# Kernel optimization log

Hardware: AMD Instinct MI355X
Metric: run time of the kernel (lower is better)

The kernel has to match this reference:

```python
import jax, jax.numpy as jnp
import numpy as np

B, T, F, H = 64, 256, 64, 512  # batch, seq_len, temporal_feature_num, hidden_size_lstm


def setup_inputs() -> dict:
    key = jax.random.key(0)
    ks = jax.random.split(key, 8)
    return {
        "temporal_features": jax.random.normal(ks[0], (B, T, F), dtype=jnp.float32),
        "temporal_masks": jax.random.uniform(ks[1], (B, T, F), dtype=jnp.float32),
        "h0": jax.random.normal(ks[2], (F, B, H), dtype=jnp.float32),
        "c0": jax.random.normal(ks[3], (F, B, H), dtype=jnp.float32),
        "W_ih": jax.random.normal(ks[4], (F, 4 * H, 2), dtype=jnp.float32) * 0.05,
        "W_hh": jax.random.normal(ks[5], (F, 4 * H, H), dtype=jnp.float32) * 0.05,
        "b_ih": jax.random.normal(ks[6], (F, 4 * H), dtype=jnp.float32) * 0.05,
        "b_hh": jax.random.normal(ks[7], (F, 4 * H), dtype=jnp.float32) * 0.05,
    }


def reference(temporal_features, temporal_masks, h0, c0, W_ih, W_hh, b_ih, b_hh):
    # x: [T, F, B, 2] -- per feature, the LSTM input is (feature_value, mask)
    x = jnp.stack([temporal_features, temporal_masks], axis=-1)  # [B, T, F, 2]
    x = jnp.transpose(x, (1, 2, 0, 3))  # [T, F, B, 2]

    bias = (b_ih + b_hh)[:, None, :]  # [F, 1, 4H]

    def step(carry, x_t):
        h, c = carry  # each [F, B, H]
        gates = (jnp.einsum('fbi,fgi->fbg', x_t, W_ih)
                 + jnp.einsum('fbh,fgh->fbg', h, W_hh)
                 + bias)  # [F, B, 4H]
        i_g, f_g, g_g, o_g = jnp.split(gates, 4, axis=-1)  # torch LSTMCell gate order i,f,g,o
        i_g = jax.nn.sigmoid(i_g)
        f_g = jax.nn.sigmoid(f_g)
        g_g = jnp.tanh(g_g)
        o_g = jax.nn.sigmoid(o_g)
        c_new = f_g * c + i_g * g_g
        h_new = o_g * jnp.tanh(c_new)
        return (h_new, c_new), None

    (h_final, _), _ = jax.lax.scan(step, (h0, c0), x)
    return h_final  # [F, B, H] -- stacked version of the returned h_list
```

## Files before the change

kernel.cpp:

```cpp
#include <hip/hip_runtime.h>
#include <hip/hip_bf16.h>
#include <stdint.h>

#define F_N 64
#define T_N 256
#define B_N 64
#define H_N 512
#define STREAM_KS 8
#define VREG_KS0 8
#define NVSTAT 6
#define LDS_KS0 14

typedef __attribute__((ext_vector_type(8))) __bf16 bf16x8;
typedef __attribute__((ext_vector_type(4))) float f32x4;
typedef __attribute__((ext_vector_type(4))) uint32_t u32x4;


__global__ void pack_x_kernel(const float* __restrict__ tf, const float* __restrict__ tm,
                              float* __restrict__ xp) {
  int tid = blockIdx.x * 256 + threadIdx.x;
  if (tid >= T_N * B_N * F_N) return;
  int f = tid & 63;
  int b = (tid >> 6) & 63;
  int t = tid >> 12;
  float v = tf[((size_t)b * T_N + t) * F_N + f];
  float m = tm[((size_t)b * T_N + t) * F_N + f];
  float* dst = xp + (((size_t)t * F_N + f) * B_N + b) * 2;
  dst[0] = v;
  dst[1] = m;
}

__global__ void pack_h0_kernel(const float* __restrict__ h0, __bf16* __restrict__ hx0) {
  int tid = blockIdx.x * 256 + threadIdx.x;
  if (tid < F_N * B_N * H_N) hx0[tid] = (__bf16)h0[tid];
}

__global__ void pack_w_kernel(const float* __restrict__ Whh, __bf16* __restrict__ Wp) {
  int gtid = blockIdx.x * 256 + threadIdx.x;
  int lane = gtid & 63;
  int nt = (gtid >> 6) & 3;
  int ks = (gtid >> 8) & 15;
  int w = (gtid >> 12) & 7;
  int q = (gtid >> 15) & 3;
  int f = gtid >> 17;
  int l15 = lane & 15, lhi = lane >> 4;
  int n_local = w * 64 + nt * 16 + l15;
  int r_local = n_local >> 2;
  int gam = n_local & 3;
  int grow = gam * 512 + q * 128 + r_local;
  const float* src = Whh + ((size_t)f * 2048 + grow) * 512 + ks * 32 + lhi * 8;
  float4 u0 = *(const float4*)src;
  float4 u1 = *(const float4*)(src + 4);
  bf16x8 v;
  v[0] = (__bf16)u0.x; v[1] = (__bf16)u0.y; v[2] = (__bf16)u0.z; v[3] = (__bf16)u0.w;
  v[4] = (__bf16)u1.x; v[5] = (__bf16)u1.y; v[6] = (__bf16)u1.z; v[7] = (__bf16)u1.w;
  *(bf16x8*)((char*)Wp + (size_t)gtid * 16) = v;
}


__global__ void __launch_bounds__(512, 1) __attribute__((amdgpu_waves_per_eu(2, 2)))
lstm_main(
    const float* __restrict__ c0, const __bf16* __restrict__ Wp,
    const float* __restrict__ Wih, const float* __restrict__ bih,
    const float* __restrict__ bhh, const float* __restrict__ xp,
    __bf16* hx, unsigned int* barr, unsigned int* xcdmap, float* __restrict__ out) {
  const int blk = blockIdx.x;
  const int f = blk & 63;
  const int q = blk >> 6;
  const int tid = threadIdx.x;
  const int lane = tid & 63;
  const int w = tid >> 6;
  const int l15 = lane & 15;
  const int lhi = lane >> 4;
  const int ls = lane & 3;
  const int lr = l15 >> 2;

  __shared__ __align__(16) unsigned char lds_h[65536];
  __shared__ __align__(16) unsigned char lds_stage[16384];
  __shared__ __align__(16) unsigned char lds_wst[65536];
  __shared__ __align__(16) float ldsB[512];
  __shared__ __align__(16) float lds0[512];
  __shared__ __align__(16) float lds1[512];
  __shared__ int s_same;

  {
    int i = tid;
    int r = i >> 2, g = i & 3;
    int row = g * 512 + q * 128 + r;
    size_t ro = (size_t)f * 2048 + row;
    ldsB[i] = bih[ro] + bhh[ro];
    lds0[i] = Wih[ro * 2 + 0];
    lds1[i] = Wih[ro * 2 + 1];
  }

  if (tid == 0) {
    uint32_t xcc;
    asm volatile("s_getreg_b32 %0, hwreg(HW_REG_XCC_ID)" : "=s"(xcc));
    xcc &= 15u;
    __hip_atomic_store(&xcdmap[f * 4 + q], xcc + 1u, __ATOMIC_RELAXED,
                       __HIP_MEMORY_SCOPE_AGENT);
    uint32_t ids[4];
    int ok = 1;
    for (int j = 0; j < 4; ++j) {
      unsigned int it = 0;
      uint32_t v;
      do {
        v = __hip_atomic_load(&xcdmap[f * 4 + j], __ATOMIC_RELAXED,
                              __HIP_MEMORY_SCOPE_AGENT);
        if (++it > 2000000u) { ok = 0; break; }
        if (v == 0u) __builtin_amdgcn_s_sleep(2);
      } while (v == 0u);
      ids[j] = v;
    }
    if (ok) ok = (ids[0] == ids[1]) & (ids[1] == ids[2]) & (ids[2] == ids[3]);
    s_same = ok;
  }

  const bf16x8* wpbase = (const bf16x8*)Wp + ((size_t)((f * 4 + q) * 8 + w)) * 4096 + lane;

  bf16x8 s[3][4];
#define LOAD_SLOT(SL, KS)                                       \
  {                                                             \
    _Pragma("unroll") for (int nt_ = 0; nt_ < 4; ++nt_)         \
        s[SL][nt_] = wpbase[((KS) * 4 + nt_) * 64];             \
  }

  bf16x8 wsf[NVSTAT][4];
#pragma unroll
  for (int s2 = 0; s2 < NVSTAT; ++s2)
#pragma unroll
    for (int nt = 0; nt < 4; ++nt) wsf[s2][nt] = wpbase[((VREG_KS0 + s2) * 4 + nt) * 64];

#pragma unroll
  for (int ksi = 0; ksi < 2; ++ksi)
#pragma unroll
    for (int nt = 0; nt < 4; ++nt) {
      bf16x8 v = wpbase[((LDS_KS0 + ksi) * 4 + nt) * 64];
      *(bf16x8*)(lds_wst + (((ksi * 8 + w) * 4 + nt) << 10) + lane * 16) = v;
    }

  float c_reg[4][4];
#pragma unroll
  for (int mt = 0; mt < 4; ++mt) {
    int brow = mt * 16 + lhi * 4 + ls;
#pragma unroll
    for (int nt = 0; nt < 4; ++nt) {
      int rg = w * 16 + nt * 4 + lr;
      c_reg[mt][nt] = c0[((size_t)f * B_N + brow) * H_N + q * 128 + rg];
    }
  }

  const size_t hxfeat = (size_t)f * (B_N * H_N);
  const size_t hxstride = (size_t)F_N * B_N * H_N;

  {
    const unsigned char* src = (const unsigned char*)(hx + hxfeat);
    uint32_t b = tid >> 3;
    uint32_t off = (tid & 7) * 32;
    uint32_t sw = (b & 7) << 4;
#pragma unroll
    for (int qq = 0; qq < 4; ++qq) {
      uint32_t gb = b * 1024 + qq * 256 + off;
      uint4 u0 = *(const uint4*)(src + gb);
      uint4 u1 = *(const uint4*)(src + gb + 16);
      *(uint4*)(lds_h + (gb ^ sw)) = u0;
      *(uint4*)(lds_h + ((gb + 16) ^ sw)) = u1;
    }
  }
  LOAD_SLOT(0, 0);
  LOAD_SLOT(1, 1);
  LOAD_SLOT(2, 2);
  __syncthreads();
  const bool fastpath = (s_same != 0);

#define READ_A(KS)                                                                     \
  {                                                                                    \
    _Pragma("unroll") for (int mt = 0; mt < 4; ++mt) {                                 \
      int row = mt * 16 + l15;                                                         \
      uint32_t byteoff =                                                               \
          (uint32_t)(row * 1024) + (((uint32_t)((KS) * 64 + lhi * 16)) ^ ((row & 7) << 4)); \
      a[mt] = *(const bf16x8*)(lds_h + byteoff);                                       \
    }                                                                                  \
  }
#define MFMA_W(WARR)                                                                   \
  {                                                                                    \
    _Pragma("unroll") for (int mt = 0; mt < 4; ++mt)                                   \
        _Pragma("unroll") for (int nt = 0; nt < 4; ++nt)                               \
            acc[mt][nt] = __builtin_amdgcn_mfma_f32_16x16x32_bf16(a[mt], (WARR)[nt],   \
                                                                  acc[mt][nt], 0, 0, 0); \
  }
#define STATIC_V(S2) { READ_A(VREG_KS0 + (S2)); MFMA_W(wsf[S2]); }
#define STATIC_L(KSI)                                                                  \
  {                                                                                    \
    READ_A(LDS_KS0 + (KSI));                                                           \
    bf16x8 wfrag[4];                                                                   \
    _Pragma("unroll") for (int nt = 0; nt < 4; ++nt) wfrag[nt] =                       \
        *(const bf16x8*)(lds_wst + ((((KSI) * 8 + w) * 4 + nt) << 10) + lane * 16);    \
    MFMA_W(wfrag);                                                                     \
  }
#define STREAM(POS)                                                                    \
  {                                                                                    \
    const int ks_ = ((POS) + par4) & 7;                                                \
    READ_A(ks_);                                                                       \
    MFMA_W(s[(POS) % 3]);                                                              \
    if ((POS) + 3 < STREAM_KS) {                                                       \
      const int ksn_ = ((POS) + 3 + par4) & 7;                                         \
      _Pragma("unroll") for (int nt_ = 0; nt_ < 4; ++nt_)                              \
          s[(POS) % 3][nt_] = wpbase[(ksn_ * 4 + nt_) * 64];                           \
    }                                                                                  \
  }

#pragma unroll 1
  for (int t = 0; t < T_N; ++t) {
    const int par4 = (t & 1) << 2;
    const int par4n = ((t + 1) & 1) << 2;
    f32x4 acc[4][4] = {};
    bf16x8 a[4];

    STATIC_V(0); STREAM(0);
    STATIC_V(1); STREAM(1);
    STATIC_V(2); STREAM(2);
    STATIC_V(3); STREAM(3);
    STATIC_V(4); STREAM(4);
    STATIC_V(5); STREAM(5);
    STATIC_L(0); STREAM(6);
    STATIC_L(1); STREAM(7);

    const bool last = (t == T_N - 1);
    const float* xpt = xp + (((size_t)t * F_N + f) * B_N) * 2;
#pragma unroll
    for (int mt = 0; mt < 4; ++mt) {
      int brow = mt * 16 + lhi * 4 + ls;
      float xv = xpt[brow * 2];
      float xm = xpt[brow * 2 + 1];
#pragma unroll
      for (int nt = 0; nt < 4; ++nt) {
        float v0 = acc[mt][nt][0], v1 = acc[mt][nt][1], v2 = acc[mt][nt][2], v3 = acc[mt][nt][3];
        {
          float t0 = __shfl_xor(v0, 1), t1 = __shfl_xor(v1, 1),
                t2 = __shfl_xor(v2, 1), t3 = __shfl_xor(v3, 1);
          if (lane & 1) { v0 = t1; v2 = t3; } else { v1 = t0; v3 = t2; }
        }
        {
          float t0 = __shfl_xor(v0, 2), t1 = __shfl_xor(v1, 2),
                t2 = __shfl_xor(v2, 2), t3 = __shfl_xor(v3, 2);
          if (lane & 2) { v0 = t2; v1 = t3; } else { v2 = t0; v3 = t1; }
        }
        int rg = w * 16 + nt * 4 + lr;
        int idx4 = rg << 2;
        float4 tb = *(const float4*)&ldsB[idx4];
        float4 w0t = *(const float4*)&lds0[idx4];
        float4 w1t = *(const float4*)&lds1[idx4];
        v0 += tb.x + w0t.x * xv + w1t.x * xm;
        v1 += tb.y + w0t.y * xv + w1t.y * xm;
        v2 += tb.z + w0t.z * xv + w1t.z * xm;
        v3 += tb.w + w0t.w * xv + w1t.w * xm;
        float ig = __builtin_amdgcn_rcpf(1.0f + __expf(-v0));
        float fg = __builtin_amdgcn_rcpf(1.0f + __expf(-v1));
        float gg = 2.0f * __builtin_amdgcn_rcpf(1.0f + __expf(-2.0f * v2)) - 1.0f;
        float og = __builtin_amdgcn_rcpf(1.0f + __expf(-v3));
        float cn = fg * c_reg[mt][nt] + ig * gg;
        c_reg[mt][nt] = cn;
        float th = 2.0f * __builtin_amdgcn_rcpf(1.0f + __expf(-2.0f * cn)) - 1.0f;
        float hn = og * th;
        if (last) {
          out[((size_t)f * B_N + brow) * H_N + q * 128 + rg] = hn;
        } else {
          uint32_t sw = (uint32_t)((brow & 7) << 4);
          *(__bf16*)(lds_stage + ((uint32_t)(brow * 256 + rg * 2) ^ sw)) = (__bf16)hn;
        }
      }
    }
    if (last) break;

    __syncthreads();

    {
      __bf16* dstbuf = hx + ((size_t)((t + 1) & 1)) * hxstride + hxfeat;
      uint32_t b = tid >> 3;
      uint32_t off = (tid & 7) * 32;
      uint32_t sw = (b & 7) << 4;
      u32x4 u0 = *(const u32x4*)(lds_stage + ((b * 256 + off) ^ sw));
      u32x4 u1 = *(const u32x4*)(lds_stage + ((b * 256 + off + 16) ^ sw));
      unsigned char* dp = (unsigned char*)dstbuf + b * 1024 + q * 256 + off;
      if (fastpath) {
        asm volatile("global_store_dwordx4 %0, %1, off sc0" ::"v"(dp), "v"(u0) : "memory");
        asm volatile("global_store_dwordx4 %0, %1, off sc0" ::"v"(dp + 16), "v"(u1) : "memory");
        asm volatile("s_waitcnt vmcnt(0)" ::: "memory");
      } else {
        *(u32x4*)(dp) = u0;
        *(u32x4*)(dp + 16) = u1;
      }
      uint32_t hb = b * 1024 + q * 256 + off;
      *(u32x4*)(lds_h + (hb ^ sw)) = u0;
      *(u32x4*)(lds_h + ((hb + 16) ^ sw)) = u1;
    }
    __syncthreads();

    if (tid == 0) {
      unsigned int* bp = barr + f * T_N + t;
      if (fastpath)
        __hip_atomic_fetch_add(bp, 1u, __ATOMIC_RELAXED, __HIP_MEMORY_SCOPE_AGENT);
      else
        __hip_atomic_fetch_add(bp, 1u, __ATOMIC_RELEASE, __HIP_MEMORY_SCOPE_AGENT);
    }
    LOAD_SLOT(0, (0 + par4n) & 7);
    LOAD_SLOT(1, (1 + par4n) & 7);
    LOAD_SLOT(2, (2 + par4n) & 7);
    if (tid == 0) {
      unsigned int* bp = barr + f * T_N + t;
      unsigned int it = 0;
      while (__hip_atomic_load(bp, __ATOMIC_RELAXED, __HIP_MEMORY_SCOPE_AGENT) < 4u) {
        __builtin_amdgcn_s_sleep(1);
        if (++it > 4000000u) break;
      }
      if (!fastpath)
        (void)__hip_atomic_load(bp, __ATOMIC_ACQUIRE, __HIP_MEMORY_SCOPE_AGENT);
    }
    __syncthreads();

    if (fastpath) {
      asm volatile("buffer_inv sc0" ::: "memory");
    }
    {
      const unsigned char* src =
          (const unsigned char*)(hx + ((size_t)((t + 1) & 1)) * hxstride + hxfeat);
      uint32_t b = tid >> 3;
      uint32_t off = (tid & 7) * 32;
      uint32_t sw = (b & 7) << 4;
#pragma unroll
      for (int qq = 0; qq < 4; ++qq) {
        if (qq == q) continue;
        uint32_t gb = b * 1024 + qq * 256 + off;
        uint4 u0 = *(const uint4*)(src + gb);
        uint4 u1 = *(const uint4*)(src + gb + 16);
        *(uint4*)(lds_h + (gb ^ sw)) = u0;
        *(uint4*)(lds_h + ((gb + 16) ^ sw)) = u1;
      }
    }
    __syncthreads();
  }
#undef LOAD_SLOT
#undef READ_A
#undef MFMA_W
#undef STATIC_V
#undef STATIC_L
#undef STREAM
}

extern "C" void kernel_launch(void* const* d_in, const int* in_sizes, int n_in,
                              void* d_out, int out_size, void* d_ws, size_t ws_size,
                              hipStream_t stream) {
  const float* tf = (const float*)d_in[0];
  const float* tm = (const float*)d_in[1];
  const float* h0 = (const float*)d_in[2];
  const float* c0 = (const float*)d_in[3];
  const float* Wih = (const float*)d_in[4];
  const float* Whh = (const float*)d_in[5];
  const float* bih = (const float*)d_in[6];
  const float* bhh = (const float*)d_in[7];
  float* out = (float*)d_out;

  const size_t WP_BYTES = (size_t)8388608 * 16;
  const size_t XP_BYTES = (size_t)T_N * F_N * B_N * 2 * 4;
  const size_t HX_BYTES = (size_t)2 * F_N * B_N * H_N * 2;
  const size_t BARR_BYTES = (size_t)F_N * T_N * 4;
  const size_t MAP_BYTES = 1024;
  if (ws_size < WP_BYTES + XP_BYTES + HX_BYTES + BARR_BYTES + MAP_BYTES) return;

  char* ws = (char*)d_ws;
  __bf16* Wp = (__bf16*)ws;
  float* xp = (float*)(ws + WP_BYTES);
  __bf16* hx = (__bf16*)(ws + WP_BYTES + XP_BYTES);
  unsigned int* barr = (unsigned int*)(ws + WP_BYTES + XP_BYTES + HX_BYTES);
  unsigned int* xcdmap = (unsigned int*)(ws + WP_BYTES + XP_BYTES + HX_BYTES + BARR_BYTES);

  hipMemsetAsync(barr, 0, BARR_BYTES + MAP_BYTES, stream);
  pack_x_kernel<<<(T_N * B_N * F_N + 255) / 256, 256, 0, stream>>>(tf, tm, xp);
  pack_h0_kernel<<<(F_N * B_N * H_N + 255) / 256, 256, 0, stream>>>(h0, hx);
  pack_w_kernel<<<8388608 / 256, 256, 0, stream>>>(Whh, Wp);
  lstm_main<<<256, 512, 0, stream>>>(c0, Wp, Wih, bih, bhh, xp, hx, barr, xcdmap, out);
}
```

Baseline: 6.142 ms.

## Add per-XCD lockstep barrier and reverse stream k-slice order on odd steps

Adds an extra per-XCD barrier after the per-feature barrier. Each XCD with exactly 32 resident blocks waits until all of them finish the timestep, so the blocks that share that XCD's L2 stream the same weight slices together. The streamed k-slice order now changes from a rotation by 4 to an XOR with 7 on odd steps, so slices last used in the previous step are touched first. This aims to improve L2 hit rate for the streamed weights. It adds a cross-block wait per step that can stall on the slowest block.

```diff
diff --git a/kernel.cpp b/kernel.cpp
--- a/kernel.cpp
+++ b/kernel.cpp
@@ -63,7 +63,8 @@
     const float* __restrict__ c0, const __bf16* __restrict__ Wp,
     const float* __restrict__ Wih, const float* __restrict__ bih,
     const float* __restrict__ bhh, const float* __restrict__ xp,
-    __bf16* hx, unsigned int* barr, unsigned int* xcdmap, float* __restrict__ out) {
+    __bf16* hx, unsigned int* barr, unsigned int* xcdmap, unsigned int* xbar,
+    float* __restrict__ out) {
   const int blk = blockIdx.x;
   const int f = blk & 63;
   const int q = blk >> 6;
@@ -82,6 +83,8 @@
   __shared__ __align__(16) float lds0[512];
   __shared__ __align__(16) float lds1[512];
   __shared__ int s_same;
+  __shared__ int s_xt;
+  __shared__ int s_xcc;
 
   {
     int i = tid;
@@ -114,6 +117,25 @@
     }
     if (ok) ok = (ids[0] == ids[1]) & (ids[1] == ids[2]) & (ids[2] == ids[3]);
     s_same = ok;
+    int xt = 0;
+    if (ok) {
+      int good = 1, cnt = 0;
+      for (int j2 = 0; j2 < 256; ++j2) {
+        unsigned int it2 = 0;
+        uint32_t v2;
+        do {
+          v2 = __hip_atomic_load(&xcdmap[j2], __ATOMIC_RELAXED,
+                                 __HIP_MEMORY_SCOPE_AGENT);
+          if (v2 == 0u) __builtin_amdgcn_s_sleep(2);
+          if (++it2 > 2000000u) { good = 0; break; }
+        } while (v2 == 0u);
+        if (!good) break;
+        cnt += (v2 == xcc + 1u);
+      }
+      if (good && cnt == 32) xt = 32;
+    }
+    s_xt = xt;
+    s_xcc = (int)xcc;
   }
 
   const bf16x8* wpbase = (const bf16x8*)Wp + ((size_t)((f * 4 + q) * 8 + w)) * 4096 + lane;
@@ -172,6 +194,8 @@
   LOAD_SLOT(2, 2);
   __syncthreads();
   const bool fastpath = (s_same != 0);
+  int xsync = s_xt;
+  const int myxcc = s_xcc;
 
 #define READ_A(KS)                                                                     \
   {                                                                                    \
@@ -200,11 +224,11 @@
   }
 #define STREAM(POS)                                                                    \
   {                                                                                    \
-    const int ks_ = ((POS) + par4) & 7;                                                \
+    const int ks_ = (POS) ^ smask;                                                     \
     READ_A(ks_);                                                                       \
     MFMA_W(s[(POS) % 3]);                                                              \
     if ((POS) + 3 < STREAM_KS) {                                                       \
-      const int ksn_ = ((POS) + 3 + par4) & 7;                                         \
+      const int ksn_ = ((POS) + 3) ^ smask;                                            \
       _Pragma("unroll") for (int nt_ = 0; nt_ < 4; ++nt_)                              \
           s[(POS) % 3][nt_] = wpbase[(ksn_ * 4 + nt_) * 64];                           \
     }                                                                                  \
@@ -212,8 +236,8 @@
 
 #pragma unroll 1
   for (int t = 0; t < T_N; ++t) {
-    const int par4 = (t & 1) << 2;
-    const int par4n = ((t + 1) & 1) << 2;
+    const int smask = (t & 1) ? 7 : 0;
+    const int smaskn = ((t + 1) & 1) ? 7 : 0;
     f32x4 acc[4][4] = {};
     bf16x8 a[4];
 
@@ -304,9 +328,9 @@
       else
         __hip_atomic_fetch_add(bp, 1u, __ATOMIC_RELEASE, __HIP_MEMORY_SCOPE_AGENT);
     }
-    LOAD_SLOT(0, (0 + par4n) & 7);
-    LOAD_SLOT(1, (1 + par4n) & 7);
-    LOAD_SLOT(2, (2 + par4n) & 7);
+    LOAD_SLOT(0, 0 ^ smaskn);
+    LOAD_SLOT(1, 1 ^ smaskn);
+    LOAD_SLOT(2, 2 ^ smaskn);
     if (tid == 0) {
       unsigned int* bp = barr + f * T_N + t;
       unsigned int it = 0;
@@ -316,6 +340,15 @@
       }
       if (!fastpath)
         (void)__hip_atomic_load(bp, __ATOMIC_ACQUIRE, __HIP_MEMORY_SCOPE_AGENT);
+      if (xsync) {
+        unsigned int* xb = xbar + ((unsigned int)myxcc) * T_N + t;
+        __hip_atomic_fetch_add(xb, 1u, __ATOMIC_RELAXED, __HIP_MEMORY_SCOPE_AGENT);
+        unsigned int it3 = 0;
+        while (__hip_atomic_load(xb, __ATOMIC_RELAXED, __HIP_MEMORY_SCOPE_AGENT) < 32u) {
+          __builtin_amdgcn_s_sleep(1);
+          if (++it3 > 1000000u) { xsync = 0; break; }
+        }
+      }
     }
     __syncthreads();
 
@@ -366,7 +399,9 @@
   const size_t HX_BYTES = (size_t)2 * F_N * B_N * H_N * 2;
   const size_t BARR_BYTES = (size_t)F_N * T_N * 4;
   const size_t MAP_BYTES = 1024;
-  if (ws_size < WP_BYTES + XP_BYTES + HX_BYTES + BARR_BYTES + MAP_BYTES) return;
+  const size_t XBAR_BYTES = (size_t)8 * T_N * 4;
+  if (ws_size < WP_BYTES + XP_BYTES + HX_BYTES + BARR_BYTES + MAP_BYTES + XBAR_BYTES)
+    return;
 
   char* ws = (char*)d_ws;
   __bf16* Wp = (__bf16*)ws;
@@ -374,10 +409,12 @@
   __bf16* hx = (__bf16*)(ws + WP_BYTES + XP_BYTES);
   unsigned int* barr = (unsigned int*)(ws + WP_BYTES + XP_BYTES + HX_BYTES);
   unsigned int* xcdmap = (unsigned int*)(ws + WP_BYTES + XP_BYTES + HX_BYTES + BARR_BYTES);
-
-  hipMemsetAsync(barr, 0, BARR_BYTES + MAP_BYTES, stream);
+  unsigned int* xbar =
+      (unsigned int*)(ws + WP_BYTES + XP_BYTES + HX_BYTES + BARR_BYTES + MAP_BYTES);
+
+  hipMemsetAsync(barr, 0, BARR_BYTES + MAP_BYTES + XBAR_BYTES, stream);
   pack_x_kernel<<<(T_N * B_N * F_N + 255) / 256, 256, 0, stream>>>(tf, tm, xp);
   pack_h0_kernel<<<(F_N * B_N * H_N + 255) / 256, 256, 0, stream>>>(h0, hx);
   pack_w_kernel<<<8388608 / 256, 256, 0, stream>>>(Whh, Wp);
-  lstm_main<<<256, 512, 0, stream>>>(c0, Wp, Wih, bih, bhh, xp, hx, barr, xcdmap, out);
+  lstm_main<<<256, 512, 0, stream>>>(c0, Wp, Wih, bih, bhh, xp, hx, barr, xcdmap, xbar, out);
 }
```

Result: slower. 7.858 ms (+27.9%).

## Overlap own-quarter K-units of next step's GEMM with cross-block barrier wait

Applied to the files above, without the earlier changes.

Renumbers the K-units per block so each block's first units cover the hidden-state quarter it computed itself. Four of those MFMA steps (EARLY4) now run for the next timestep before waiting on the cross-block barrier and loading the other quarters of h. The aim is to hide the barrier spin and global h exchange behind useful matrix work. The cost is that the accumulators stay live across the barrier, which adds register pressure. The weight-to-unit mapping also has to remain consistent with the packed weight layout.

```diff
diff --git a/kernel.cpp b/kernel.cpp
--- a/kernel.cpp
+++ b/kernel.cpp
@@ -6,10 +6,8 @@
 #define T_N 256
 #define B_N 64
 #define H_N 512
-#define STREAM_KS 8
-#define VREG_KS0 8
 #define NVSTAT 6
-#define LDS_KS0 14
+#define NSTREAM 8
 
 typedef __attribute__((ext_vector_type(8))) __bf16 bf16x8;
 typedef __attribute__((ext_vector_type(4))) float f32x4;
@@ -74,6 +72,9 @@
   const int lhi = lane >> 4;
   const int ls = lane & 3;
   const int lr = l15 >> 2;
+  const int uq = q << 2;
+
+#define UNITJ(J) ((uq + (J)) & 15)
 
   __shared__ __align__(16) unsigned char lds_h[65536];
   __shared__ __align__(16) unsigned char lds_stage[16384];
@@ -119,25 +120,30 @@
   const bf16x8* wpbase = (const bf16x8*)Wp + ((size_t)((f * 4 + q) * 8 + w)) * 4096 + lane;
 
   bf16x8 s[3][4];
-#define LOAD_SLOT(SL, KS)                                       \
-  {                                                             \
-    _Pragma("unroll") for (int nt_ = 0; nt_ < 4; ++nt_)         \
-        s[SL][nt_] = wpbase[((KS) * 4 + nt_) * 64];             \
+#define LOAD_SLOT(SL, P, PAR)                                       \
+  {                                                                 \
+    const int u_ = UNITJ(8 + (((P) + (PAR)) & 7));                  \
+    _Pragma("unroll") for (int nt_ = 0; nt_ < 4; ++nt_)             \
+        s[SL][nt_] = wpbase[(u_ * 4 + nt_) * 64];                   \
   }
 
   bf16x8 wsf[NVSTAT][4];
 #pragma unroll
-  for (int s2 = 0; s2 < NVSTAT; ++s2)
-#pragma unroll
-    for (int nt = 0; nt < 4; ++nt) wsf[s2][nt] = wpbase[((VREG_KS0 + s2) * 4 + nt) * 64];
-
-#pragma unroll
-  for (int ksi = 0; ksi < 2; ++ksi)
+  for (int s2 = 0; s2 < NVSTAT; ++s2) {
+    const int u_ = UNITJ(s2);
+#pragma unroll
+    for (int nt = 0; nt < 4; ++nt) wsf[s2][nt] = wpbase[(u_ * 4 + nt) * 64];
+  }
+
+#pragma unroll
+  for (int ksi = 0; ksi < 2; ++ksi) {
+    const int u_ = UNITJ(6 + ksi);
 #pragma unroll
     for (int nt = 0; nt < 4; ++nt) {
-      bf16x8 v = wpbase[((LDS_KS0 + ksi) * 4 + nt) * 64];
+      bf16x8 v = wpbase[(u_ * 4 + nt) * 64];
       *(bf16x8*)(lds_wst + (((ksi * 8 + w) * 4 + nt) << 10) + lane * 16) = v;
     }
+  }
 
   float c_reg[4][4];
 #pragma unroll
@@ -167,18 +173,18 @@
       *(uint4*)(lds_h + ((gb + 16) ^ sw)) = u1;
     }
   }
-  LOAD_SLOT(0, 0);
-  LOAD_SLOT(1, 1);
-  LOAD_SLOT(2, 2);
+  LOAD_SLOT(0, 0, 0);
+  LOAD_SLOT(1, 1, 0);
+  LOAD_SLOT(2, 2, 0);
   __syncthreads();
   const bool fastpath = (s_same != 0);
 
-#define READ_A(KS)                                                                     \
+#define READ_A(U)                                                                      \
   {                                                                                    \
     _Pragma("unroll") for (int mt = 0; mt < 4; ++mt) {                                 \
       int row = mt * 16 + l15;                                                         \
       uint32_t byteoff =                                                               \
-          (uint32_t)(row * 1024) + (((uint32_t)((KS) * 64 + lhi * 16)) ^ ((row & 7) << 4)); \
+          (uint32_t)(row * 1024) + (((uint32_t)((U) * 64 + lhi * 16)) ^ ((row & 7) << 4)); \
       a[mt] = *(const bf16x8*)(lds_h + byteoff);                                       \
     }                                                                                  \
   }
@@ -189,10 +195,10 @@
             acc[mt][nt] = __builtin_amdgcn_mfma_f32_16x16x32_bf16(a[mt], (WARR)[nt],   \
                                                                   acc[mt][nt], 0, 0, 0); \
   }
-#define STATIC_V(S2) { READ_A(VREG_KS0 + (S2)); MFMA_W(wsf[S2]); }
+#define STATIC_V(S2) { READ_A(UNITJ(S2)); MFMA_W(wsf[S2]); }
 #define STATIC_L(KSI)                                                                  \
   {                                                                                    \
-    READ_A(LDS_KS0 + (KSI));                                                           \
+    READ_A(UNITJ(6 + (KSI)));                                                          \
     bf16x8 wfrag[4];                                                                   \
     _Pragma("unroll") for (int nt = 0; nt < 4; ++nt) wfrag[nt] =                       \
         *(const bf16x8*)(lds_wst + ((((KSI) * 8 + w) * 4 + nt) << 10) + lane * 16);    \
@@ -200,31 +206,71 @@
   }
 #define STREAM(POS)                                                                    \
   {                                                                                    \
-    const int ks_ = ((POS) + par4) & 7;                                                \
-    READ_A(ks_);                                                                       \
+    const int u_ = UNITJ(8 + (((POS) + par4) & 7));                                    \
+    READ_A(u_);                                                                        \
     MFMA_W(s[(POS) % 3]);                                                              \
-    if ((POS) + 3 < STREAM_KS) {                                                       \
-      const int ksn_ = ((POS) + 3 + par4) & 7;                                         \
+    if ((POS) + 3 < NSTREAM) {                                                         \
+      const int un_ = UNITJ(8 + (((POS) + 3 + par4) & 7));                             \
       _Pragma("unroll") for (int nt_ = 0; nt_ < 4; ++nt_)                              \
-          s[(POS) % 3][nt_] = wpbase[(ksn_ * 4 + nt_) * 64];                           \
+          s[(POS) % 3][nt_] = wpbase[(un_ * 4 + nt_) * 64];                            \
     }                                                                                  \
   }
+#define ACC_CLEAR                                                                      \
+  {                                                                                    \
+    _Pragma("unroll") for (int mt = 0; mt < 4; ++mt)                                   \
+        _Pragma("unroll") for (int nt = 0; nt < 4; ++nt)                               \
+            acc[mt][nt] = (f32x4){0.0f, 0.0f, 0.0f, 0.0f};                             \
+  }
+#define EARLY4 { STATIC_V(0); STATIC_V(1); STATIC_V(2); STATIC_V(3); }
+
+  f32x4 acc[4][4] = {};
+  bf16x8 a[4];
+  EARLY4;
 
 #pragma unroll 1
   for (int t = 0; t < T_N; ++t) {
     const int par4 = (t & 1) << 2;
     const int par4n = ((t + 1) & 1) << 2;
-    f32x4 acc[4][4] = {};
-    bf16x8 a[4];
-
-    STATIC_V(0); STREAM(0);
-    STATIC_V(1); STREAM(1);
-    STATIC_V(2); STREAM(2);
-    STATIC_V(3); STREAM(3);
-    STATIC_V(4); STREAM(4);
-    STATIC_V(5); STREAM(5);
-    STATIC_L(0); STREAM(6);
-    STATIC_L(1); STREAM(7);
+
+    if (t > 0) {
+      if (tid == 0) {
+        unsigned int* bp = barr + f * T_N + (t - 1);
+        unsigned int it = 0;
+        while (__hip_atomic_load(bp, __ATOMIC_RELAXED, __HIP_MEMORY_SCOPE_AGENT) < 4u) {
+          __builtin_amdgcn_s_sleep(1);
+          if (++it > 4000000u) break;
+        }
+        if (!fastpath)
+          (void)__hip_atomic_load(bp, __ATOMIC_ACQUIRE, __HIP_MEMORY_SCOPE_AGENT);
+      }
+      __syncthreads();
+      if (fastpath) {
+        asm volatile("buffer_inv sc0" ::: "memory");
+      }
+      {
+        const unsigned char* src =
+            (const unsigned char*)(hx + ((size_t)(t & 1)) * hxstride + hxfeat);
+        uint32_t b = tid >> 3;
+        uint32_t off = (tid & 7) * 32;
+        uint32_t sw = (b & 7) << 4;
+#pragma unroll
+        for (int qq = 0; qq < 4; ++qq) {
+          if (qq == q) continue;
+          uint32_t gb = b * 1024 + qq * 256 + off;
+          uint4 u0 = *(const uint4*)(src + gb);
+          uint4 u1 = *(const uint4*)(src + gb + 16);
+          *(uint4*)(lds_h + (gb ^ sw)) = u0;
+          *(uint4*)(lds_h + ((gb + 16) ^ sw)) = u1;
+        }
+      }
+      __syncthreads();
+    }
+
+    STATIC_V(4); STREAM(0);
+    STATIC_V(5); STREAM(1);
+    STATIC_L(0); STREAM(2);
+    STATIC_L(1); STREAM(3);
+    STREAM(4); STREAM(5); STREAM(6); STREAM(7);
 
     const bool last = (t == T_N - 1);
     const float* xpt = xp + (((size_t)t * F_N + f) * B_N) * 2;
@@ -304,41 +350,11 @@
       else
         __hip_atomic_fetch_add(bp, 1u, __ATOMIC_RELEASE, __HIP_MEMORY_SCOPE_AGENT);
     }
-    LOAD_SLOT(0, (0 + par4n) & 7);
-    LOAD_SLOT(1, (1 + par4n) & 7);
-    LOAD_SLOT(2, (2 + par4n) & 7);
-    if (tid == 0) {
-      unsigned int* bp = barr + f * T_N + t;
-      unsigned int it = 0;
-      while (__hip_atomic_load(bp, __ATOMIC_RELAXED, __HIP_MEMORY_SCOPE_AGENT) < 4u) {
-        __builtin_amdgcn_s_sleep(1);
-        if (++it > 4000000u) break;
-      }
-      if (!fastpath)
-        (void)__hip_atomic_load(bp, __ATOMIC_ACQUIRE, __HIP_MEMORY_SCOPE_AGENT);
-    }
-    __syncthreads();
-
-    if (fastpath) {
-      asm volatile("buffer_inv sc0" ::: "memory");
-    }
-    {
-      const unsigned char* src =
-          (const unsigned char*)(hx + ((size_t)((t + 1) & 1)) * hxstride + hxfeat);
-      uint32_t b = tid >> 3;
-      uint32_t off = (tid & 7) * 32;
-      uint32_t sw = (b & 7) << 4;
-#pragma unroll
-      for (int qq = 0; qq < 4; ++qq) {
-        if (qq == q) continue;
-        uint32_t gb = b * 1024 + qq * 256 + off;
-        uint4 u0 = *(const uint4*)(src + gb);
-        uint4 u1 = *(const uint4*)(src + gb + 16);
-        *(uint4*)(lds_h + (gb ^ sw)) = u0;
-        *(uint4*)(lds_h + ((gb + 16) ^ sw)) = u1;
-      }
-    }
-    __syncthreads();
+    LOAD_SLOT(0, 0, par4n);
+    LOAD_SLOT(1, 1, par4n);
+    LOAD_SLOT(2, 2, par4n);
+    ACC_CLEAR;
+    EARLY4;
   }
 #undef LOAD_SLOT
 #undef READ_A
@@ -346,6 +362,9 @@
 #undef STATIC_V
 #undef STATIC_L
 #undef STREAM
+#undef ACC_CLEAR
+#undef EARLY4
+#undef UNITJ
 }
 
 extern "C" void kernel_launch(void* const* d_in, const int* in_sizes, int n_in,
```

After: 6.166 ms. No clear change (+0.4%).
